# Performance work log

Measured on AMD Instinct MI355X. Metric: run time of the kernel, lower is better.

The kernel has to match this reference:

```python
import jax, jax.numpy as jnp
import numpy as np

# dims: T=tgt_len, B=batch, A=n_agents, S=src_len, V=vocab, N_OOV=out-of-vocab slots
T, B, A, S, V, N_OOV = 64, 8, 3, 400, 50000, 400
V_EXT = V + N_OOV


def setup_inputs() -> dict:
    key = jax.random.key(0)
    k1, k2, k3, k4, k5 = jax.random.split(key, 5)
    article = jax.random.randint(k1, (S, B, A), 0, V_EXT)
    vocab_probs = jax.nn.softmax(jax.random.normal(k2, (T, B, V), dtype=jnp.float32), axis=-1)
    generation_probs = jax.nn.sigmoid(jax.random.normal(k3, (T, B, A), dtype=jnp.float32))
    agentwise_attn = jax.nn.softmax(jax.random.normal(k4, (T, B, A, S), dtype=jnp.float32), axis=-1)
    agent_attn = jax.nn.softmax(jax.random.normal(k5, (T, B, A), dtype=jnp.float32), axis=-1)
    return {"article": article, "vocab_probs": vocab_probs,
            "generation_probs": generation_probs, "agentwise_attn": agentwise_attn,
            "agent_attn": agent_attn}


def reference(article, vocab_probs, generation_probs, agentwise_attn, agent_attn):
    # pointer-generator mix, per (t, b, agent)
    gen = generation_probs[..., None]                      # [T,B,A,1]
    voc_gen = gen * vocab_probs[:, :, None, :]             # [T,B,A,V]
    copy_w = (1.0 - gen) * agentwise_attn                  # [T,B,A,S]
    # scatter_add copy weights into extended vocab at article token ids
    idx = jnp.transpose(article, (1, 2, 0))                # [B,A,S]
    idx = jnp.broadcast_to(idx[None], (T, B, A, S)).reshape(T * B * A, S)
    ext = jnp.zeros((T * B * A, V_EXT), vocab_probs.dtype)
    ext = ext.at[jnp.arange(T * B * A)[:, None], idx].add(copy_w.reshape(T * B * A, S))
    ext = ext.reshape(T, B, A, V_EXT)
    ext = ext.at[..., :V].add(voc_gen)                     # generation part on base vocab
    # weighted sum over agents -> [T,B,V_EXT]
    return jnp.einsum('tba,tbav->tbv', agent_attn, ext)
```

## Files before the change

kernel.cpp:

```cpp
#include <hip/hip_runtime.h>

constexpr int T = 64, B = 8, A = 3, S = 400, V = 50000, N_OOV = 400;
constexpr int V_EXT  = V + N_OOV;
constexpr int NSUB   = 6;
constexpr int C_SUB  = V_EXT / NSUB;
constexpr int C4_SUB = C_SUB / 4;
constexpr int V4     = V / 4;
constexpr int NTHR   = 512;
constexpr int FULL_K = C4_SUB / NTHR;
constexpr int NSC    = 3;

typedef float vfloat4 __attribute__((ext_vector_type(4)));

__global__ __launch_bounds__(NTHR, 8) void pg_async_kernel(
    const int*   __restrict__ article,
    const float* __restrict__ vocab_probs,
    const float* __restrict__ gen_probs,
    const float* __restrict__ agentwise_attn,
    const float* __restrict__ agent_attn,
    float*       __restrict__ out)
{
    __shared__ float acc[C_SUB];
    const int bid = blockIdx.x;
    const int tb  = bid / NSUB;
    const int sub = bid - tb * NSUB;
    const int b   = tb % B;
    const int tid = threadIdx.x;

    float coef = 0.f;
    float cw[A];
#pragma unroll
    for (int a = 0; a < A; ++a) {
        const float aa = agent_attn[tb * A + a];
        const float g  = gen_probs[tb * A + a];
        coef += aa * g;
        cw[a] = aa * (1.f - g);
    }

    int   sidx[NSC];
    float sraw[NSC];
    const float* aw = agentwise_attn + (size_t)tb * A * S;
#pragma unroll
    for (int j = 0; j < NSC; ++j) {
        const int i2 = tid + j * NTHR;
        sidx[j] = -1; sraw[j] = 0.f;
        if (i2 < A * S) {
            const int a = (i2 >= 2 * S) ? 2 : (i2 >= S ? 1 : 0);
            const int s = i2 - a * S;
            sidx[j] = article[(s * B + b) * A + a];
            sraw[j] = aw[i2];
        }
    }

    const float4* vp4  = reinterpret_cast<const float4*>(vocab_probs + (size_t)tb * V);
    vfloat4*      out4 = reinterpret_cast<vfloat4*>(out + (size_t)tb * V_EXT);
    const int base = sub * C4_SUB;
    const int i0   = base + tid;

    float4 v[FULL_K];
#pragma unroll
    for (int k = 0; k < FULL_K; ++k) {
        const int i  = i0 + k * NTHR;
        const int ic = (i < V4) ? i : (V4 - 1);
        v[k] = vp4[ic];
    }
    const int  it       = i0 + FULL_K * NTHR;
    const bool has_tail = (it < base + C4_SUB);
    float4 vt = make_float4(0.f, 0.f, 0.f, 0.f);
    if (has_tail) vt = vp4[(it < V4) ? it : (V4 - 1)];

    __builtin_amdgcn_sched_barrier(0);

    float4* acc4 = reinterpret_cast<float4*>(acc);
    for (int j = tid; j < C4_SUB; j += NTHR)
        acc4[j] = make_float4(0.f, 0.f, 0.f, 0.f);

    asm volatile("s_waitcnt lgkmcnt(0)" ::: "memory");
    __builtin_amdgcn_s_barrier();
    __builtin_amdgcn_sched_barrier(0);

    const int lo = sub * C_SUB;
    const int hi = lo + C_SUB;
#pragma unroll
    for (int j = 0; j < NSC; ++j) {
        if (sidx[j] >= lo && sidx[j] < hi) {
            const int i2 = tid + j * NTHR;
            const int a  = (i2 >= 2 * S) ? 2 : (i2 >= S ? 1 : 0);
            atomicAdd(&acc[sidx[j] - lo], cw[a] * sraw[j]);
        }
    }

    asm volatile("s_waitcnt lgkmcnt(0)" ::: "memory");
    __builtin_amdgcn_s_barrier();
    __builtin_amdgcn_sched_barrier(0);

#pragma unroll
    for (int k = 0; k < FULL_K; ++k) {
        const int i = i0 + k * NTHR;
        float4 r = acc4[i - base];
        if (i < V4) {
            r.x += coef * v[k].x;  r.y += coef * v[k].y;
            r.z += coef * v[k].z;  r.w += coef * v[k].w;
        }
        vfloat4 rr = {r.x, r.y, r.z, r.w};
        __builtin_nontemporal_store(rr, &out4[i]);
    }
    if (has_tail) {
        float4 r = acc4[it - base];
        if (it < V4) {
            r.x += coef * vt.x;  r.y += coef * vt.y;
            r.z += coef * vt.z;  r.w += coef * vt.w;
        }
        vfloat4 rr = {r.x, r.y, r.z, r.w};
        __builtin_nontemporal_store(rr, &out4[it]);
    }
}

extern "C" void kernel_launch(void* const* d_in, const int* in_sizes, int n_in,
                              void* d_out, int out_size, void* d_ws, size_t ws_size,
                              hipStream_t stream) {
    const int*   article        = (const int*)  d_in[0];
    const float* vocab_probs    = (const float*)d_in[1];
    const float* gen_probs      = (const float*)d_in[2];
    const float* agentwise_attn = (const float*)d_in[3];
    const float* agent_attn     = (const float*)d_in[4];
    float*       out            = (float*)d_out;

    pg_async_kernel<<<dim3(T * B * NSUB), dim3(NTHR), 0, stream>>>(
        article, vocab_probs, gen_probs, agentwise_attn, agent_attn, out);
}
```

Baseline: 37.66 us.

## Process three vocab sub-chunks per block with fewer, longer-lived blocks

Result: slower. 38.69 us (+2.7%).

```diff
diff --git a/kernel.cpp b/kernel.cpp
--- a/kernel.cpp
+++ b/kernel.cpp
@@ -9,10 +9,9 @@
 constexpr int NTHR   = 512;
 constexpr int FULL_K = C4_SUB / NTHR;
 constexpr int NSC    = 3;
+constexpr int NBLK   = T * B * NSUB / 3;
 
-typedef float vfloat4 __attribute__((ext_vector_type(4)));
-
-__global__ __launch_bounds__(NTHR, 8) void pg_async_kernel(
+__global__ __launch_bounds__(NTHR, 8) void pg_persist_kernel(
     const int*   __restrict__ article,
     const float* __restrict__ vocab_probs,
     const float* __restrict__ gen_probs,
@@ -21,11 +20,11 @@
     float*       __restrict__ out)
 {
     __shared__ float acc[C_SUB];
-    const int bid = blockIdx.x;
-    const int tb  = bid / NSUB;
-    const int sub = bid - tb * NSUB;
-    const int b   = tb % B;
-    const int tid = threadIdx.x;
+    const int blk  = blockIdx.x;
+    const int tb   = blk >> 1;
+    const int half = blk & 1;
+    const int b    = tb % B;
+    const int tid  = threadIdx.x;
 
     float coef = 0.f;
     float cw[A];
@@ -38,81 +37,94 @@
     }
 
     int   sidx[NSC];
-    float sraw[NSC];
+    float sw[NSC];
     const float* aw = agentwise_attn + (size_t)tb * A * S;
 #pragma unroll
     for (int j = 0; j < NSC; ++j) {
         const int i2 = tid + j * NTHR;
-        sidx[j] = -1; sraw[j] = 0.f;
+        sidx[j] = -1; sw[j] = 0.f;
         if (i2 < A * S) {
             const int a = (i2 >= 2 * S) ? 2 : (i2 >= S ? 1 : 0);
             const int s = i2 - a * S;
             sidx[j] = article[(s * B + b) * A + a];
-            sraw[j] = aw[i2];
+            sw[j]   = cw[a] * aw[i2];
         }
     }
 
+    float4* acc4 = reinterpret_cast<float4*>(acc);
     const float4* vp4  = reinterpret_cast<const float4*>(vocab_probs + (size_t)tb * V);
-    vfloat4*      out4 = reinterpret_cast<vfloat4*>(out + (size_t)tb * V_EXT);
-    const int base = sub * C4_SUB;
-    const int i0   = base + tid;
+    float4*       out4 = reinterpret_cast<float4*>(out + (size_t)tb * V_EXT);
 
-    float4 v[FULL_K];
-#pragma unroll
-    for (int k = 0; k < FULL_K; ++k) {
-        const int i  = i0 + k * NTHR;
-        const int ic = (i < V4) ? i : (V4 - 1);
-        v[k] = vp4[ic];
-    }
-    const int  it       = i0 + FULL_K * NTHR;
-    const bool has_tail = (it < base + C4_SUB);
-    float4 vt = make_float4(0.f, 0.f, 0.f, 0.f);
-    if (has_tail) vt = vp4[(it < V4) ? it : (V4 - 1)];
-
-    __builtin_amdgcn_sched_barrier(0);
-
-    float4* acc4 = reinterpret_cast<float4*>(acc);
     for (int j = tid; j < C4_SUB; j += NTHR)
         acc4[j] = make_float4(0.f, 0.f, 0.f, 0.f);
-
+    asm volatile("s_waitcnt lgkmcnt(0)" ::: "memory");
+    __builtin_amdgcn_s_barrier();
+    __builtin_amdgcn_sched_barrier(0);
+    {
+        const int lo = (half * 3) * C_SUB;
+#pragma unroll
+        for (int j = 0; j < NSC; ++j)
+            if (sidx[j] >= lo && sidx[j] < lo + C_SUB)
+                atomicAdd(&acc[sidx[j] - lo], sw[j]);
+    }
     asm volatile("s_waitcnt lgkmcnt(0)" ::: "memory");
     __builtin_amdgcn_s_barrier();
     __builtin_amdgcn_sched_barrier(0);
 
-    const int lo = sub * C_SUB;
-    const int hi = lo + C_SUB;
+    for (int u = 0; u < 3; ++u) {
+        const int sub  = half * 3 + u;
+        const int base = sub * C4_SUB;
+        const int i0   = base + tid;
+
+        float4 v[FULL_K];
 #pragma unroll
-    for (int j = 0; j < NSC; ++j) {
-        if (sidx[j] >= lo && sidx[j] < hi) {
-            const int i2 = tid + j * NTHR;
-            const int a  = (i2 >= 2 * S) ? 2 : (i2 >= S ? 1 : 0);
-            atomicAdd(&acc[sidx[j] - lo], cw[a] * sraw[j]);
+        for (int k = 0; k < FULL_K; ++k) {
+            const int i  = i0 + k * NTHR;
+            const int ic = (i < V4) ? i : (V4 - 1);
+            v[k] = vp4[ic];
         }
-    }
-
-    asm volatile("s_waitcnt lgkmcnt(0)" ::: "memory");
-    __builtin_amdgcn_s_barrier();
-    __builtin_amdgcn_sched_barrier(0);
+        const int  it       = i0 + FULL_K * NTHR;
+        const bool has_tail = (it < base + C4_SUB);
+        float4 vt = make_float4(0.f, 0.f, 0.f, 0.f);
+        if (has_tail) vt = vp4[(it < V4) ? it : (V4 - 1)];
 
 #pragma unroll
-    for (int k = 0; k < FULL_K; ++k) {
-        const int i = i0 + k * NTHR;
-        float4 r = acc4[i - base];
-        if (i < V4) {
-            r.x += coef * v[k].x;  r.y += coef * v[k].y;
-            r.z += coef * v[k].z;  r.w += coef * v[k].w;
+        for (int k = 0; k < FULL_K; ++k) {
+            const int i = i0 + k * NTHR;
+            float4 r = acc4[i - base];
+            if (i < V4) {
+                r.x += coef * v[k].x;  r.y += coef * v[k].y;
+                r.z += coef * v[k].z;  r.w += coef * v[k].w;
+            }
+            out4[i] = r;
         }
-        vfloat4 rr = {r.x, r.y, r.z, r.w};
-        __builtin_nontemporal_store(rr, &out4[i]);
-    }
-    if (has_tail) {
-        float4 r = acc4[it - base];
-        if (it < V4) {
-            r.x += coef * vt.x;  r.y += coef * vt.y;
-            r.z += coef * vt.z;  r.w += coef * vt.w;
+        if (has_tail) {
+            float4 r = acc4[it - base];
+            if (it < V4) {
+                r.x += coef * vt.x;  r.y += coef * vt.y;
+                r.z += coef * vt.z;  r.w += coef * vt.w;
+            }
+            out4[it] = r;
         }
-        vfloat4 rr = {r.x, r.y, r.z, r.w};
-        __builtin_nontemporal_store(rr, &out4[it]);
+
+        if (u < 2) {
+            asm volatile("s_waitcnt lgkmcnt(0)" ::: "memory");
+            __builtin_amdgcn_s_barrier();
+            __builtin_amdgcn_sched_barrier(0);
+            for (int j = tid; j < C4_SUB; j += NTHR)
+                acc4[j] = make_float4(0.f, 0.f, 0.f, 0.f);
+            asm volatile("s_waitcnt lgkmcnt(0)" ::: "memory");
+            __builtin_amdgcn_s_barrier();
+            __builtin_amdgcn_sched_barrier(0);
+            const int lo = (sub + 1) * C_SUB;
+#pragma unroll
+            for (int j = 0; j < NSC; ++j)
+                if (sidx[j] >= lo && sidx[j] < lo + C_SUB)
+                    atomicAdd(&acc[sidx[j] - lo], sw[j]);
+            asm volatile("s_waitcnt lgkmcnt(0)" ::: "memory");
+            __builtin_amdgcn_s_barrier();
+            __builtin_amdgcn_sched_barrier(0);
+        }
     }
 }
 
@@ -126,6 +138,6 @@
     const float* agent_attn     = (const float*)d_in[4];
     float*       out            = (float*)d_out;
 
-    pg_async_kernel<<<dim3(T * B * NSUB), dim3(NTHR), 0, stream>>>(
+    pg_persist_kernel<<<dim3(NBLK), dim3(NTHR), 0, stream>>>(
         article, vocab_probs, gen_probs, agentwise_attn, agent_attn, out);
 }
```
